# Optimization experiments

Measured on AMD Instinct MI355X. Metric: run time of the kernel, lower is better.

Reference implementation:

```python
import jax, jax.numpy as jnp
import numpy as np

B, S, D, H = 2, 2048, 1024, 16
DK = D // H  # 64
EPS = 1e-5


def setup_inputs() -> dict:
    key = jax.random.key(0)
    ks = jax.random.split(key, 12)
    sc = 1.0 / np.sqrt(D)
    inp = {
        "Q": jax.random.normal(ks[0], (B, S, D), jnp.float32),
        "K": jax.random.normal(ks[1], (B, S, D), jnp.float32),
        "V": jax.random.normal(ks[2], (B, S, D), jnp.float32),
        # causal mask: True = masked out
        "attn_mask": jnp.broadcast_to(jnp.triu(jnp.ones((S, S), bool), k=1), (B, S, S)),
        # torch Linear weights stored [out, in]
        "Wq": jax.random.normal(ks[3], (D, D), jnp.float32) * sc,
        "bq": jnp.zeros((D,), jnp.float32),
        "Wk": jax.random.normal(ks[4], (D, D), jnp.float32) * sc,
        "bk": jnp.zeros((D,), jnp.float32),
        "Wv": jax.random.normal(ks[5], (D, D), jnp.float32) * sc,
        "bv": jnp.zeros((D,), jnp.float32),
        "Wo": jax.random.normal(ks[6], (D, D), jnp.float32) * sc,
        "bo": jnp.zeros((D,), jnp.float32),
        "gamma": jnp.ones((D,), jnp.float32),
        "beta": jnp.zeros((D,), jnp.float32),
    }
    return inp


def _layer_norm(x, gamma, beta):
    mu = jnp.mean(x, axis=-1, keepdims=True)
    var = jnp.mean(jnp.square(x - mu), axis=-1, keepdims=True)
    return (x - mu) * jax.lax.rsqrt(var + EPS) * gamma + beta


def reference(Q, K, V, attn_mask, Wq, bq, Wk, bk, Wv, bv, Wo, bo, gamma, beta):
    residual = Q
    # projections -> [B, H, S, DK]
    q = (Q @ Wq.T + bq).reshape(B, S, H, DK).transpose(0, 2, 1, 3)
    k = (K @ Wk.T + bk).reshape(B, S, H, DK).transpose(0, 2, 1, 3)
    v = (V @ Wv.T + bv).reshape(B, S, H, DK).transpose(0, 2, 1, 3)
    scores = jnp.einsum("bhqd,bhkd->bhqk", q, k) / np.sqrt(DK)
    scores = jnp.where(attn_mask[:, None, :, :], -1e9, scores)
    attn = jax.nn.softmax(scores, axis=-1)
    ctx = jnp.einsum("bhqk,bhkd->bhqd", attn, v)  # [B,H,S,DK]
    ctx = ctx.transpose(0, 2, 1, 3).reshape(B, S, H * DK)
    out = ctx @ Wo.T + bo
    return _layer_norm(out + residual, gamma, beta), attn
```

## Files before the change

### kernel.cpp

```cpp
#include <hip/hip_runtime.h>
#include <hip/hip_fp16.h>

#define BB 2
#define SS 2048
#define DD 1024
#define HH 16
#define DKK 64
#define BHH (BB*HH)
#define MM (BB*SS)
#define EPSF 1e-5f

typedef _Float16 f16;
typedef _Float16 f16x4 __attribute__((ext_vector_type(4)));
typedef _Float16 f16x8 __attribute__((ext_vector_type(8)));
typedef float f32x4 __attribute__((ext_vector_type(4)));

__device__ __forceinline__ int swz128(int row, int byteInRow) {
    return row * 128 + (byteInRow ^ ((row & 7) << 4));
}

__device__ __forceinline__ void gl_lds16(const f16* g, f16* l) {
    __builtin_amdgcn_global_load_lds((const __attribute__((address_space(1))) void*)g,
                                     (__attribute__((address_space(3))) void*)l, 16, 0, 0);
}

__global__ __launch_bounds__(256) void cvt_pass(
    const float* __restrict__ s0, const float* __restrict__ s1, const float* __restrict__ s2,
    const float* __restrict__ s3, const float* __restrict__ s4, const float* __restrict__ s5,
    const float* __restrict__ s6,
    f16* __restrict__ d0, f16* __restrict__ d1, f16* __restrict__ d2,
    f16* __restrict__ d3, f16* __restrict__ d4, f16* __restrict__ d5, f16* __restrict__ d6)
{
    const int y = blockIdx.y;
    const float* s; f16* d; int n4;
    switch (y) {
        case 0: s = s0; d = d0; n4 = (MM * DD) / 4; break;
        case 1: s = s1; d = d1; n4 = (MM * DD) / 4; break;
        case 2: s = s2; d = d2; n4 = (MM * DD) / 4; break;
        case 3: s = s3; d = d3; n4 = (DD * DD) / 4; break;
        case 4: s = s4; d = d4; n4 = (DD * DD) / 4; break;
        case 5: s = s5; d = d5; n4 = (DD * DD) / 4; break;
        default: s = s6; d = d6; n4 = (DD * DD) / 4; break;
    }
    for (int i = blockIdx.x * 256 + threadIdx.x; i < n4; i += 256 * 256) {
        f32x4 v = ((const f32x4*)s)[i];
        f16x4 h = { (f16)v.x, (f16)v.y, (f16)v.z, (f16)v.w };
        ((f16x4*)d)[i] = h;
    }
}

__global__ __launch_bounds__(256) void qkv_gemm(
    const f16* __restrict__ Qf, const f16* __restrict__ Kf, const f16* __restrict__ Vf,
    const f16* __restrict__ Wqf, const float* __restrict__ bq,
    const f16* __restrict__ Wkf, const float* __restrict__ bk,
    const f16* __restrict__ Wvf, const float* __restrict__ bv,
    f16* __restrict__ qh, f16* __restrict__ kh, f16* __restrict__ vTh)
{
    const int type = blockIdx.z;
    const f16* X = (type == 0) ? Qf : (type == 1) ? Kf : Vf;
    const f16* W = (type == 0) ? Wqf : (type == 1) ? Wkf : Wvf;
    const float* bias = (type == 0) ? bq : (type == 1) ? bk : bv;
    const int m0 = blockIdx.y * 128, n0 = blockIdx.x * 128;

    __shared__ f16 a_lds[2][128 * 64];
    __shared__ f16 b_lds[2][128 * 64];

    const int t = threadIdx.x;
    const int l = t & 63, w = t >> 6;
    const int wr = (w >> 1) * 64, wc = (w & 1) * 64;

    f32x4 acc[4][4] = {};

    #define QKV_STAGE(kt, buf) { \
        _Pragma("unroll") \
        for (int p = 0; p < 4; p++) { \
            int idx = w * 4 + p; \
            int gci = idx * 64 + l; \
            int row = gci >> 3, slot = gci & 7; \
            int ss = slot ^ (row & 7); \
            gl_lds16(X + (size_t)(m0 + row) * DD + (kt) * 64 + ss * 8, a_lds[buf] + idx * 512); \
            gl_lds16(W + (size_t)(n0 + row) * DD + (kt) * 64 + ss * 8, b_lds[buf] + idx * 512); \
        } }

    QKV_STAGE(0, 0);
    for (int k0 = 0; k0 < 16; k0++) {
        asm volatile("s_waitcnt vmcnt(0)");
        __builtin_amdgcn_s_barrier();
        __builtin_amdgcn_sched_barrier(0);
        if (k0 + 1 < 16) QKV_STAGE(k0 + 1, (k0 + 1) & 1);
        const f16* al = a_lds[k0 & 1];
        const f16* bl = b_lds[k0 & 1];
        #pragma unroll
        for (int kk = 0; kk < 2; kk++) {
            f16x8 af[4], bf[4];
            #pragma unroll
            for (int mi = 0; mi < 4; mi++) {
                int row = wr + mi * 16 + (l & 15);
                af[mi] = *(const f16x8*)((const char*)al + swz128(row, kk * 64 + (l >> 4) * 16));
            }
            #pragma unroll
            for (int ni = 0; ni < 4; ni++) {
                int row = wc + ni * 16 + (l & 15);
                bf[ni] = *(const f16x8*)((const char*)bl + swz128(row, kk * 64 + (l >> 4) * 16));
            }
            __builtin_amdgcn_s_setprio(1);
            #pragma unroll
            for (int mi = 0; mi < 4; mi++)
                #pragma unroll
                for (int ni = 0; ni < 4; ni++)
                    acc[mi][ni] = __builtin_amdgcn_mfma_f32_16x16x32_f16(af[mi], bf[ni], acc[mi][ni], 0, 0, 0);
            __builtin_amdgcn_s_setprio(0);
        }
    }
    #undef QKV_STAGE

    if (type == 2) {
        __syncthreads();
        f16* tb = (f16*)a_lds;
        #pragma unroll
        for (int mi = 0; mi < 4; mi++) {
            #pragma unroll
            for (int ni = 0; ni < 4; ni++) {
                int nl = wc + ni * 16 + (l & 15);
                int mb = (wr + mi * 16 + (l >> 4) * 4) * 2;
                f16x4 hv;
                #pragma unroll
                for (int r = 0; r < 4; r++)
                    hv[r] = (f16)(acc[mi][ni][r] + bias[n0 + nl]);
                *(f16x4*)((char*)tb + nl * 256 + (mb ^ ((nl & 7) << 4))) = hv;
            }
        }
        __syncthreads();
        const int b = m0 >> 11;
        const int mloc = m0 & (SS - 1);
        #pragma unroll
        for (int i = 0; i < 8; i++) {
            int o = w * 8192 + i * 1024 + l * 16;
            int nl = o >> 8;
            int inb = o & 255;
            f16x8 v = *(const f16x8*)((char*)tb + nl * 256 + (inb ^ ((nl & 7) << 4)));
            int ng = n0 + nl, h_ = ng >> 6, dk = ng & 63;
            int s = mloc + inb / 2;
            *(f16x8*)(vTh + ((size_t)((b * HH + h_) * DKK + dk)) * SS + s) = v;
        }
    } else {
        #pragma unroll
        for (int mi = 0; mi < 4; mi++) {
            #pragma unroll
            for (int ni = 0; ni < 4; ni++) {
                #pragma unroll
                for (int r = 0; r < 4; r++) {
                    int m = m0 + wr + mi * 16 + (l >> 4) * 4 + r;
                    int n = n0 + wc + ni * 16 + (l & 15);
                    float v = acc[mi][ni][r] + bias[n];
                    f16 hv = (f16)v;
                    int b = m >> 11, s = m & (SS - 1);
                    int h_ = n >> 6, dk = n & (DKK - 1);
                    f16* dst = (type == 0) ? qh : kh;
                    dst[((size_t)((b * HH + h_) * SS + s)) * DKK + dk] = hv;
                }
            }
        }
    }
}

__global__ __launch_bounds__(256) void attn_kernel(
    const f16* __restrict__ qh, const f16* __restrict__ kh, const f16* __restrict__ vTh,
    float* __restrict__ attn_out, f16* __restrict__ ctx)
{
    const int bid = blockIdx.x;
    const int swz = (bid & 7) * 128 + (bid >> 3);
    const int bh = swz >> 5;
    const int qb = 31 - (swz & 31);
    const int qbase = qb * 64;
    const int t = threadIdx.x, l = t & 63, w = t >> 6;
    const int c = l & 15, g = l >> 4;

    __shared__ f16 kb3[3][64 * 64];
    __shared__ f16 vb3[3][64 * 64];

    const float CSC = 0.125f * 1.44269504f;
    const int nj = qb + 1;
    const int qloc = w * 16 + c;
    const int qglob = qbase + qloc;

    const f16* kbase = kh + (size_t)bh * SS * DKK;
    const f16* vbase = vTh + (size_t)bh * DKK * SS;
    float* aout = attn_out + (size_t)bh * SS * SS;

    const f16* qsrc = qh + (size_t)bh * SS * DKK + (size_t)qglob * DKK;
    f16x8 bq[2];
    bq[0] = *(const f16x8*)(qsrc + g * 8);
    bq[1] = *(const f16x8*)(qsrc + 32 + g * 8);

    #define STAGE_K(jt, buf) { \
        const f16* ksrc_ = kbase + (size_t)(jt) * 64 * DKK; \
        _Pragma("unroll") \
        for (int p = 0; p < 2; p++) { \
            int idx = w * 2 + p; \
            int gci = idx * 64 + l; \
            int row = gci >> 3, slot = gci & 7; \
            int ss_ = slot ^ (row & 7); \
            gl_lds16(ksrc_ + row * DKK + ss_ * 8, kb3[buf] + idx * 512); \
        } }
    #define STAGE_V(jt, buf) { \
        const f16* vsrc_ = vbase + (size_t)(jt) * 64; \
        _Pragma("unroll") \
        for (int p = 0; p < 2; p++) { \
            int idx = w * 2 + p; \
            int gci = idx * 64 + l; \
            int row = gci >> 3, slot = gci & 7; \
            int ss_ = slot ^ (row & 7); \
            gl_lds16(vsrc_ + (size_t)row * SS + ss_ * 8, vb3[buf] + idx * 512); \
        } }

    #define QKT(dstf, srcb) { \
        __builtin_amdgcn_s_setprio(1); \
        _Pragma("unroll") \
        for (int dw = 0; dw < 2; dw++) { \
            _Pragma("unroll") \
            for (int ni = 0; ni < 4; ni++) { \
                f16x8 ak = *(const f16x8*)((const char*)(srcb) + swz128(ni * 16 + c, dw * 64 + g * 16)); \
                dstf[ni] = __builtin_amdgcn_mfma_f32_16x16x32_f16(ak, bq[dw], dstf[ni], 0, 0, 0); \
            } \
        } \
        __builtin_amdgcn_s_setprio(0); }

    #define PSTORE(jt) { \
        float* pl_ = (float*)vb3; \
        _Pragma("unroll") \
        for (int i = 0; i < 4; i++) { \
            int row_ = w * 16 + 4 * i + g; \
            f32x4 v_ = *(const f32x4*)((char*)pl_ + row_ * 256 + ((c * 16) ^ ((row_ & 7) << 4))); \
            __builtin_nontemporal_store(v_, (f32x4*)(aout + (size_t)(qbase + row_) * SS + (jt) * 64 + c * 4)); \
        } }

    #define CBAR(n) { asm volatile("s_waitcnt vmcnt(" #n ")"); \
                      __builtin_amdgcn_s_barrier(); \
                      __builtin_amdgcn_sched_barrier(0); }

    STAGE_K(0, 0);
    if (nj > 1) STAGE_K(1, 1);
    STAGE_V(0, 0);
    CBAR(0);

    float lrow = 0.f;
    f32x4 cacc[4] = {};
    f32x4 sprev[4];

    for (int j = 0; j < nj; j++) {
        if (j + 2 < nj) STAGE_K(j + 2, (j + 2) % 3);
        if (j + 1 < nj) STAGE_V(j + 1, (j + 1) % 3);

        f32x4 scur[4] = {};
        QKT(scur, kb3[j % 3]);

        if (j > 0) {
            const f16* pvv = vb3[(j - 1) % 3];
            f16x4 bfr[4];
            #pragma unroll
            for (int ni = 0; ni < 4; ni++) {
                float e0 = exp2f(sprev[ni][0] * CSC);
                float e1 = exp2f(sprev[ni][1] * CSC);
                float e2 = exp2f(sprev[ni][2] * CSC);
                float e3 = exp2f(sprev[ni][3] * CSC);
                lrow += e0 + e1 + e2 + e3;
                bfr[ni] = f16x4{ (f16)e0, (f16)e1, (f16)e2, (f16)e3 };
            }
            __builtin_amdgcn_s_setprio(1);
            #pragma unroll
            for (int ni2 = 0; ni2 < 4; ni2++) {
                #pragma unroll
                for (int nk = 0; nk < 4; nk++) {
                    f16x4 av = *(const f16x4*)((const char*)pvv + swz128(ni2 * 16 + c, nk * 32 + g * 8));
                    cacc[ni2] = __builtin_amdgcn_mfma_f32_16x16x16f16(av, bfr[nk], cacc[ni2], 0, 0, 0);
                }
            }
            __builtin_amdgcn_s_setprio(0);
        }

        if (j + 3 <= nj)      CBAR(4)
        else if (j + 2 == nj) CBAR(2)
        else                  CBAR(0);

        #pragma unroll
        for (int x = 0; x < 4; x++) sprev[x] = scur[x];
    }

    STAGE_K(0, 0);
    if (nj > 1) STAGE_K(1, 1);

    {
        const f16* pvv = vb3[(nj - 1) % 3];
        f16x4 bfr[4];
        #pragma unroll
        for (int ni = 0; ni < 4; ni++) {
            int kkb = ni * 16 + 4 * g;
            float e0 = (kkb + 0 > qloc) ? 0.f : exp2f(sprev[ni][0] * CSC);
            float e1 = (kkb + 1 > qloc) ? 0.f : exp2f(sprev[ni][1] * CSC);
            float e2 = (kkb + 2 > qloc) ? 0.f : exp2f(sprev[ni][2] * CSC);
            float e3 = (kkb + 3 > qloc) ? 0.f : exp2f(sprev[ni][3] * CSC);
            lrow += e0 + e1 + e2 + e3;
            bfr[ni] = f16x4{ (f16)e0, (f16)e1, (f16)e2, (f16)e3 };
        }
        __builtin_amdgcn_s_setprio(1);
        #pragma unroll
        for (int ni2 = 0; ni2 < 4; ni2++) {
            #pragma unroll
            for (int nk = 0; nk < 4; nk++) {
                f16x4 av = *(const f16x4*)((const char*)pvv + swz128(ni2 * 16 + c, nk * 32 + g * 8));
                cacc[ni2] = __builtin_amdgcn_mfma_f32_16x16x16f16(av, bfr[nk], cacc[ni2], 0, 0, 0);
            }
        }
        __builtin_amdgcn_s_setprio(0);
    }

    lrow += __shfl_xor(lrow, 16);
    lrow += __shfl_xor(lrow, 32);
    const float rinv = 1.f / lrow;
    const float nls = -__log2f(lrow);

    {
        int b = bh >> 4, h_ = bh & 15;
        f16* cbase = ctx + (size_t)(b * SS + qglob) * DD + h_ * 64;
        #pragma unroll
        for (int ni2 = 0; ni2 < 4; ni2++) {
            f16x4 hv = { (f16)(cacc[ni2][0] * rinv), (f16)(cacc[ni2][1] * rinv),
                         (f16)(cacc[ni2][2] * rinv), (f16)(cacc[ni2][3] * rinv) };
            *(f16x4*)(cbase + ni2 * 16 + 4 * g) = hv;
        }
    }

    CBAR(0);

    {
        float* pl = (float*)vb3;
        for (int j = 0; j < nj; j++) {
            if (j + 2 < nj) STAGE_K(j + 2, (j + 2) % 3);

            f32x4 scur[4] = {};
            QKT(scur, kb3[j % 3]);

            if (j > 0) {
                #pragma unroll
                for (int ni = 0; ni < 4; ni++) {
                    f32x4 st = { exp2f(fmaf(sprev[ni][0], CSC, nls)),
                                 exp2f(fmaf(sprev[ni][1], CSC, nls)),
                                 exp2f(fmaf(sprev[ni][2], CSC, nls)),
                                 exp2f(fmaf(sprev[ni][3], CSC, nls)) };
                    *(f32x4*)((char*)pl + (w * 16 + c) * 256 + ((ni * 64 + g * 16) ^ ((c & 7) << 4))) = st;
                }
                PSTORE(j - 1);
            }

            if (j == 0 && j + 2 < nj)  CBAR(2)
            else if (j + 2 < nj)       CBAR(6)
            else if (j > 0)            CBAR(4)
            else                       CBAR(0);

            #pragma unroll
            for (int x = 0; x < 4; x++) sprev[x] = scur[x];
        }

        {
            #pragma unroll
            for (int ni = 0; ni < 4; ni++) {
                int kkb = ni * 16 + 4 * g;
                f32x4 st = { (kkb + 0 > qloc) ? 0.f : exp2f(fmaf(sprev[ni][0], CSC, nls)),
                             (kkb + 1 > qloc) ? 0.f : exp2f(fmaf(sprev[ni][1], CSC, nls)),
                             (kkb + 2 > qloc) ? 0.f : exp2f(fmaf(sprev[ni][2], CSC, nls)),
                             (kkb + 3 > qloc) ? 0.f : exp2f(fmaf(sprev[ni][3], CSC, nls)) };
                *(f32x4*)((char*)pl + (w * 16 + c) * 256 + ((ni * 64 + g * 16) ^ ((c & 7) << 4))) = st;
            }
            PSTORE(nj - 1);
        }
    }

    {
        f32x4 z = { 0.f, 0.f, 0.f, 0.f };
        for (int jb = qb + 1; jb < 32; jb++) {
            #pragma unroll
            for (int i = 0; i < 4; i++) {
                int c2 = t + 256 * i;
                int row = c2 >> 4, cg = c2 & 15;
                __builtin_nontemporal_store(z, (f32x4*)(aout + (size_t)(qbase + row) * SS + jb * 64 + cg * 4));
            }
        }
    }
    #undef STAGE_K
    #undef STAGE_V
    #undef QKT
    #undef PSTORE
    #undef CBAR
}

__global__ __launch_bounds__(256) void oproj_gemm(
    const f16* __restrict__ A, const f16* __restrict__ Wof, const float* __restrict__ bo,
    const float* __restrict__ resid, float* __restrict__ out)
{
    const int m0 = blockIdx.y * 128, n0 = blockIdx.x * 128;
    __shared__ f16 a_lds[2][128 * 64];
    __shared__ f16 b_lds[2][128 * 64];
    const int t = threadIdx.x;
    const int l = t & 63, w = t >> 6;
    const int wr = (w >> 1) * 64, wc = (w & 1) * 64;

    f32x4 acc[4][4] = {};

    #define OP_STAGE(kt, buf) { \
        _Pragma("unroll") \
        for (int p = 0; p < 4; p++) { \
            int idx = w * 4 + p; \
            int gci = idx * 64 + l; \
            int row = gci >> 3, slot = gci & 7; \
            int ss = slot ^ (row & 7); \
            gl_lds16(A + (size_t)(m0 + row) * DD + (kt) * 64 + ss * 8, a_lds[buf] + idx * 512); \
            gl_lds16(Wof + (size_t)(n0 + row) * DD + (kt) * 64 + ss * 8, b_lds[buf] + idx * 512); \
        } }

    OP_STAGE(0, 0);
    for (int k0 = 0; k0 < 16; k0++) {
        asm volatile("s_waitcnt vmcnt(0)");
        __builtin_amdgcn_s_barrier();
        __builtin_amdgcn_sched_barrier(0);
        if (k0 + 1 < 16) OP_STAGE(k0 + 1, (k0 + 1) & 1);
        const f16* al = a_lds[k0 & 1];
        const f16* bl = b_lds[k0 & 1];
        #pragma unroll
        for (int kk = 0; kk < 2; kk++) {
            f16x8 af[4], bf[4];
            #pragma unroll
            for (int mi = 0; mi < 4; mi++) {
                int row = wr + mi * 16 + (l & 15);
                af[mi] = *(const f16x8*)((const char*)al + swz128(row, kk * 64 + (l >> 4) * 16));
            }
            #pragma unroll
            for (int ni = 0; ni < 4; ni++) {
                int row = wc + ni * 16 + (l & 15);
                bf[ni] = *(const f16x8*)((const char*)bl + swz128(row, kk * 64 + (l >> 4) * 16));
            }
            __builtin_amdgcn_s_setprio(1);
            #pragma unroll
            for (int mi = 0; mi < 4; mi++)
                #pragma unroll
                for (int ni = 0; ni < 4; ni++)
                    acc[mi][ni] = __builtin_amdgcn_mfma_f32_16x16x32_f16(af[mi], bf[ni], acc[mi][ni], 0, 0, 0);
            __builtin_amdgcn_s_setprio(0);
        }
    }
    #undef OP_STAGE

    #pragma unroll
    for (int mi = 0; mi < 4; mi++) {
        #pragma unroll
        for (int ni = 0; ni < 4; ni++) {
            #pragma unroll
            for (int r = 0; r < 4; r++) {
                int m = m0 + wr + mi * 16 + (l >> 4) * 4 + r;
                int n = n0 + wc + ni * 16 + (l & 15);
                float v = acc[mi][ni][r] + bo[n] + resid[(size_t)m * DD + n];
                out[(size_t)m * DD + n] = v;
            }
        }
    }
}

__global__ __launch_bounds__(256) void ln_kernel(
    const float* __restrict__ x, const float* __restrict__ gamma,
    const float* __restrict__ beta, float* __restrict__ out)
{
    int row = blockIdx.x;
    int t = threadIdx.x;
    float4 v = ((const float4*)(x + (size_t)row * DD))[t];
    float s = v.x + v.y + v.z + v.w;
    __shared__ float red[4];
    #pragma unroll
    for (int o = 32; o; o >>= 1) s += __shfl_down(s, o, 64);
    if ((t & 63) == 0) red[t >> 6] = s;
    __syncthreads();
    float mean = (red[0] + red[1] + red[2] + red[3]) * (1.f / DD);
    __syncthreads();
    float4 d;
    d.x = v.x - mean; d.y = v.y - mean; d.z = v.z - mean; d.w = v.w - mean;
    float q = d.x * d.x + d.y * d.y + d.z * d.z + d.w * d.w;
    #pragma unroll
    for (int o = 32; o; o >>= 1) q += __shfl_down(q, o, 64);
    if ((t & 63) == 0) red[t >> 6] = q;
    __syncthreads();
    float var = (red[0] + red[1] + red[2] + red[3]) * (1.f / DD);
    float rstd = rsqrtf(var + EPSF);
    float4 g = ((const float4*)gamma)[t];
    float4 bt = ((const float4*)beta)[t];
    float4 o4;
    o4.x = d.x * rstd * g.x + bt.x;
    o4.y = d.y * rstd * g.y + bt.y;
    o4.z = d.z * rstd * g.z + bt.z;
    o4.w = d.w * rstd * g.w + bt.w;
    ((float4*)(out + (size_t)row * DD))[t] = o4;
}

extern "C" void kernel_launch(void* const* d_in, const int* in_sizes, int n_in,
                              void* d_out, int out_size, void* d_ws, size_t ws_size,
                              hipStream_t stream)
{
    const float* Q     = (const float*)d_in[0];
    const float* K     = (const float*)d_in[1];
    const float* V     = (const float*)d_in[2];
    const float* Wq    = (const float*)d_in[4];
    const float* bq    = (const float*)d_in[5];
    const float* Wk    = (const float*)d_in[6];
    const float* bk    = (const float*)d_in[7];
    const float* Wv    = (const float*)d_in[8];
    const float* bv    = (const float*)d_in[9];
    const float* Wo    = (const float*)d_in[10];
    const float* bo    = (const float*)d_in[11];
    const float* gamma = (const float*)d_in[12];
    const float* beta  = (const float*)d_in[13];

    float* out_ln   = (float*)d_out;
    float* attn_out = (float*)d_out + (size_t)BB * SS * DD;

    f16* Qf  = (f16*)attn_out;
    f16* Kf  = Qf + (size_t)MM * DD;
    f16* Vf  = Kf + (size_t)MM * DD;
    f16* Wqf = (f16*)out_ln;
    f16* Wkf = Wqf + (size_t)DD * DD;
    f16* Wvf = Wkf + (size_t)DD * DD;
    f16* Wof = Wvf + (size_t)DD * DD;

    char* ws = (char*)d_ws;
    f16*   qh    = (f16*)(ws);
    f16*   kh    = (f16*)(ws + ((size_t)8  << 20));
    f16*   vTh   = (f16*)(ws + ((size_t)16 << 20));
    f16*   ctx   = (f16*)(ws + ((size_t)24 << 20));
    float* oproj = (float*)(ws + ((size_t)32 << 20));

    cvt_pass<<<dim3(256, 7), 256, 0, stream>>>(Q, K, V, Wq, Wk, Wv, Wo,
                                               Qf, Kf, Vf, Wqf, Wkf, Wvf, Wof);
    qkv_gemm<<<dim3(8, 32, 3), 256, 0, stream>>>(Qf, Kf, Vf, Wqf, bq, Wkf, bk, Wvf, bv, qh, kh, vTh);
    attn_kernel<<<dim3(1024), 256, 0, stream>>>(qh, kh, vTh, attn_out, ctx);
    oproj_gemm<<<dim3(8, 32), 256, 0, stream>>>(ctx, Wof, bo, Q, oproj);
    ln_kernel<<<dim3(MM), 256, 0, stream>>>(oproj, gamma, beta, out_ln);
}
```

Before: 213.2 us.

## Move causal upper-triangle zero stores from attention into GEMM kernel tails

Writing zeros to the masked upper triangle of the attention-probability output is a large pure-store workload. Most of it moves out of the attention kernel and into the tails of the QKV projection GEMM (heads 2-21) and the output-projection GEMM (heads 22-31). Heads 0-1 stay in the attention kernel because their memory is reused as scratch for the fp16 Q/K/V copies read by the QKV GEMM. The aim is to overlap bandwidth-bound zero stores with compute-bound GEMM blocks. In exchange, each GEMM block does extra strided store work after its main loop, which can lengthen the GEMMs.

```diff
diff --git a/kernel.cpp b/kernel.cpp
--- a/kernel.cpp
+++ b/kernel.cpp
@@ -22,6 +22,22 @@
 __device__ __forceinline__ void gl_lds16(const f16* g, f16* l) {
     __builtin_amdgcn_global_load_lds((const __attribute__((address_space(1))) void*)g,
                                      (__attribute__((address_space(3))) void*)l, 16, 0, 0);
+}
+
+__device__ __forceinline__ void zero_tails(float* __restrict__ attn_out,
+                                           int bh0, int nbh, int slice, int nslices, int t)
+{
+    const int total = nbh * SS;
+    f32x4 z = { 0.f, 0.f, 0.f, 0.f };
+    for (int u = slice; u < total; u += nslices) {
+        int bh = bh0 + (u >> 11);
+        int q = u & (SS - 1);
+        int cstart = ((q >> 6) + 1) << 6;
+        if (cstart >= SS) continue;
+        float* row = attn_out + (size_t)bh * SS * SS + (size_t)q * SS;
+        for (int x = cstart + t * 4; x < SS; x += 1024)
+            __builtin_nontemporal_store(z, (f32x4*)(row + x));
+    }
 }
 
 __global__ __launch_bounds__(256) void cvt_pass(
@@ -54,7 +70,8 @@
     const f16* __restrict__ Wqf, const float* __restrict__ bq,
     const f16* __restrict__ Wkf, const float* __restrict__ bk,
     const f16* __restrict__ Wvf, const float* __restrict__ bv,
-    f16* __restrict__ qh, f16* __restrict__ kh, f16* __restrict__ vTh)
+    f16* __restrict__ qh, f16* __restrict__ kh, f16* __restrict__ vTh,
+    float* __restrict__ attn_out)
 {
     const int type = blockIdx.z;
     const f16* X = (type == 0) ? Qf : (type == 1) ? Kf : Vf;
@@ -161,6 +178,11 @@
                 }
             }
         }
+    }
+
+    {
+        int slice = (blockIdx.z * 32 + blockIdx.y) * 8 + blockIdx.x;
+        zero_tails(attn_out, 2, 20, slice, 768, t);
     }
 }
 
@@ -376,7 +398,7 @@
         }
     }
 
-    {
+    if (bh < 2) {
         f32x4 z = { 0.f, 0.f, 0.f, 0.f };
         for (int jb = qb + 1; jb < 32; jb++) {
             #pragma unroll
@@ -396,7 +418,7 @@
 
 __global__ __launch_bounds__(256) void oproj_gemm(
     const f16* __restrict__ A, const f16* __restrict__ Wof, const float* __restrict__ bo,
-    const float* __restrict__ resid, float* __restrict__ out)
+    const float* __restrict__ resid, float* __restrict__ out, float* __restrict__ attn_out)
 {
     const int m0 = blockIdx.y * 128, n0 = blockIdx.x * 128;
     __shared__ f16 a_lds[2][128 * 64];
@@ -462,6 +484,11 @@
                 out[(size_t)m * DD + n] = v;
             }
         }
+    }
+
+    {
+        int slice = blockIdx.y * 8 + blockIdx.x;
+        zero_tails(attn_out, 22, 10, slice, 256, t);
     }
 }
 
@@ -537,8 +564,9 @@
 
     cvt_pass<<<dim3(256, 7), 256, 0, stream>>>(Q, K, V, Wq, Wk, Wv, Wo,
                                                Qf, Kf, Vf, Wqf, Wkf, Wvf, Wof);
-    qkv_gemm<<<dim3(8, 32, 3), 256, 0, stream>>>(Qf, Kf, Vf, Wqf, bq, Wkf, bk, Wvf, bv, qh, kh, vTh);
+    qkv_gemm<<<dim3(8, 32, 3), 256, 0, stream>>>(Qf, Kf, Vf, Wqf, bq, Wkf, bk, Wvf, bv,
+                                                 qh, kh, vTh, attn_out);
     attn_kernel<<<dim3(1024), 256, 0, stream>>>(qh, kh, vTh, attn_out, ctx);
-    oproj_gemm<<<dim3(8, 32), 256, 0, stream>>>(ctx, Wof, bo, Q, oproj);
+    oproj_gemm<<<dim3(8, 32), 256, 0, stream>>>(ctx, Wof, bo, Q, oproj, attn_out);
     ln_kernel<<<dim3(MM), 256, 0, stream>>>(oproj, gamma, beta, out_ln);
 }
```

New measurement: 234.1 us. +9.8%, slower.
